# Performance work log

Hardware: AMD Instinct MI355X
Metric: run time of the kernel (lower is better)

The kernel has to match this reference:

```python
import jax, jax.numpy as jnp
import numpy as np

N_NODES = 100000
N_EDGES = 1600000
IN_CH = 128
OUT_CH = 128


def setup_inputs() -> dict:
    key = jax.random.key(0)
    k = jax.random.split(key, 6)
    x = jax.random.normal(k[0], (N_NODES, IN_CH), dtype=jnp.float32)
    edge_index = jax.random.randint(k[1], (2, N_EDGES), 0, N_NODES, dtype=jnp.int32)
    # GCNConv linear weights (glorot-ish scale) and biases
    W1 = jax.random.normal(k[2], (IN_CH, OUT_CH), dtype=jnp.float32) / np.sqrt(IN_CH)
    b1 = jnp.zeros((OUT_CH,), dtype=jnp.float32)
    W2 = jax.random.normal(k[3], (OUT_CH, OUT_CH), dtype=jnp.float32) / np.sqrt(OUT_CH)
    b2 = jnp.zeros((OUT_CH,), dtype=jnp.float32)
    return {"x": x, "edge_index": edge_index, "W1": W1, "b1": b1, "W2": W2, "b2": b2}


def gcn_conv(x, src, dst, W, b, n_nodes):
    """PyG GCNConv: add self-loops, symmetric D^-1/2 A D^-1/2 normalization."""
    h = x @ W  # [N, out]
    # degree including the implicit self-loop (weight 1)
    ones = jnp.ones(src.shape[0], dtype=x.dtype)
    deg = jax.ops.segment_sum(ones, dst, num_segments=n_nodes) + 1.0  # [N]
    dinv = jax.lax.rsqrt(deg)  # deg >= 1 so always finite
    coef = dinv[src] * dinv[dst]  # [E] edge norm 1/sqrt(d_i d_j)
    msg = h[src] * coef[:, None]  # [E, out] gather + scale
    agg = jax.ops.segment_sum(msg, dst, num_segments=n_nodes)  # scatter-add
    # self-loop contribution: norm = dinv[i]^2
    agg = agg + h * (dinv * dinv)[:, None]
    return agg + b


def reference(x, edge_index, W1, b1, W2, b2):
    src, dst = edge_index[0], edge_index[1]
    h = jax.nn.relu(gcn_conv(x, src, dst, W1, b1, N_NODES))
    out = jax.nn.relu(gcn_conv(h, src, dst, W2, b2, N_NODES))
    return out
```

## Files before the change

kernel.cpp:

```cpp
#include <hip/hip_runtime.h>


#define NN 100000
#define NBKT 512
#define BKT_W 196
#define CHUNK 8192
#define CAP 6144

typedef __attribute__((ext_vector_type(8))) short bf16x8;
typedef __attribute__((ext_vector_type(4))) float f32x4;

__device__ __forceinline__ ushort f2bf(float f) {
  unsigned u = __float_as_uint(f);
  unsigned r = (u + 0x7fffu + ((u >> 16) & 1u)) >> 16;
  return (ushort)r;
}
__device__ __forceinline__ float bflo(unsigned p) {
  return __uint_as_float(p << 16);
}
__device__ __forceinline__ float bfhi(unsigned p) {
  return __uint_as_float(p & 0xffff0000u);
}
__device__ __forceinline__ unsigned hipair(unsigned ue, unsigned uo) {
  return (uo & 0xffff0000u) | (ue >> 16);
}


__global__ __launch_bounds__(512) void kb_hist(const int* __restrict__ dst,
                                               int* __restrict__ bcnt, int E) {
  __shared__ int h[NBKT];
  for (int i = threadIdx.x; i < NBKT; i += 512) h[i] = 0;
  __syncthreads();
  int base = blockIdx.x * CHUNK;
#pragma unroll 4
  for (int q = 0; q < CHUNK / 512; q++) {
    int e = base + threadIdx.x + q * 512;
    if (e < E) atomicAdd(&h[dst[e] / BKT_W], 1);
  }
  __syncthreads();
  for (int i = threadIdx.x; i < NBKT; i += 512)
    if (h[i]) atomicAdd(&bcnt[i], h[i]);
}

__global__ __launch_bounds__(512) void kb_scan(const int* __restrict__ bcnt,
                                               int* __restrict__ bbase,
                                               int* __restrict__ bcur,
                                               int* __restrict__ row_ptr,
                                               int N, int E) {
  __shared__ int s[NBKT];
  int t = threadIdx.x;
  int v = bcnt[t];
  s[t] = v;
  __syncthreads();
  for (int off = 1; off < NBKT; off <<= 1) {
    int x = (t >= off) ? s[t - off] : 0;
    __syncthreads();
    s[t] += x;
    __syncthreads();
  }
  int ex = s[t] - v;
  bbase[t] = ex;
  bcur[t] = ex;
  if (t == NBKT - 1) bbase[NBKT] = E;
  if (t == 0) row_ptr[N] = E;
}

__global__ __launch_bounds__(512) void kb_scatter(const int* __restrict__ src,
                                                  const int* __restrict__ dst,
                                                  int* __restrict__ bcur,
                                                  int2* __restrict__ pairs, int E) {
  __shared__ int h[NBKT];
  __shared__ int gb[NBKT];
  for (int i = threadIdx.x; i < NBKT; i += 512) h[i] = 0;
  __syncthreads();

  const int base = blockIdx.x * CHUNK;
  const int t = threadIdx.x;
  int rank[CHUNK / 512], bkt[CHUNK / 512], sv[CHUNK / 512], dv[CHUNK / 512];
#pragma unroll
  for (int q = 0; q < CHUNK / 512; q++) {
    int e = base + t + q * 512;
    if (e < E) {
      int d = dst[e];
      int b = d / BKT_W;
      bkt[q] = b;
      sv[q] = src[e];
      dv[q] = d;
      rank[q] = atomicAdd(&h[b], 1);
    } else {
      bkt[q] = -1;
    }
  }
  __syncthreads();
  for (int i = t; i < NBKT; i += 512) {
    int c = h[i];
    gb[i] = c ? atomicAdd(&bcur[i], c) : 0;
  }
  __syncthreads();
#pragma unroll
  for (int q = 0; q < CHUNK / 512; q++) {
    if (bkt[q] >= 0) pairs[(size_t)gb[bkt[q]] + rank[q]] = make_int2(sv[q], dv[q]);
  }
}

__global__ __launch_bounds__(512) void kb_sort(const int* __restrict__ bbase,
                                               const int2* __restrict__ pairs,
                                               int* __restrict__ csr_src,
                                               int* __restrict__ row_ptr,
                                               float* __restrict__ dinv,
                                               int N, int E) {
  __shared__ int cnt[256];
  __shared__ int sc[256];
  __shared__ int cur[256];
  __shared__ int stage[CAP];

  const int b = blockIdx.x;
  const int t = threadIdx.x;
  const int lo = bbase[b], hi = bbase[b + 1];
  const int n0 = b * BKT_W;
  int m = hi - lo;
  if (m > CAP) m = CAP;

  if (t < 256) cnt[t] = 0;
  __syncthreads();

  for (int i = t; i < m; i += 512) {
    int2 p = pairs[(size_t)lo + i];
    atomicAdd(&cnt[p.y - n0], 1);
  }
  __syncthreads();

  int v = 0;
  if (t < 256) {
    v = cnt[t];
    sc[t] = v;
  }
  __syncthreads();
  for (int off = 1; off < 256; off <<= 1) {
    int x = 0;
    if (t < 256 && t >= off) x = sc[t - off];
    __syncthreads();
    if (t < 256) sc[t] += x;
    __syncthreads();
  }
  if (t < 256) {
    int ex = sc[t] - v;
    cur[t] = ex;
    int node = n0 + t;
    if (t < BKT_W && node < N) {
      row_ptr[node] = lo + ex;
      dinv[node] = rsqrtf((float)v + 1.0f);
    }
  }
  __syncthreads();

  for (int i = t; i < m; i += 512) {
    int2 p = pairs[(size_t)lo + i];
    int pos = atomicAdd(&cur[p.y - n0], 1);
    stage[pos] = p.x;
  }
  __syncthreads();

  for (int i = t; i < m; i += 512) csr_src[(size_t)lo + i] = stage[i];
}

__global__ __launch_bounds__(256) void k_wsplit2(const float* __restrict__ W1,
                                                 const float* __restrict__ W2,
                                                 ushort* __restrict__ w1hi,
                                                 ushort* __restrict__ w1lo,
                                                 ushort* __restrict__ w2hi,
                                                 ushort* __restrict__ w2lo) {
  const float* W = blockIdx.x ? W2 : W1;
  ushort* whi = blockIdx.x ? w2hi : w1hi;
  ushort* wlo = blockIdx.x ? w2lo : w1lo;
  const int t = threadIdx.x;
#pragma unroll
  for (int it = 0; it < 16; ++it) {
    int f4 = it * 256 + t;
    int k = f4 >> 5;
    int n4 = (f4 & 31) * 4;
    float4 v = *(const float4*)(W + (size_t)k * 128 + n4);
    float f[4] = {v.x, v.y, v.z, v.w};
#pragma unroll
    for (int q = 0; q < 4; ++q) {
      int n = n4 + q;
      unsigned u = __float_as_uint(f[q]);
      float lf = f[q] - __uint_as_float(u & 0xffff0000u);
      int bo = (n * 256 + k * 2) ^ ((n & 7) << 4);
      *(ushort*)((char*)whi + bo) = (ushort)(u >> 16);
      *(ushort*)((char*)wlo + bo) = (ushort)(__float_as_uint(lf) >> 16);
    }
  }
}

__device__ __forceinline__ void cvt_row(const float* __restrict__ p,
                                        bf16x8* hi, bf16x8* lo) {
  float4 v0 = *(const float4*)p;
  float4 v1 = *(const float4*)(p + 4);
  float f[8] = {v0.x, v0.y, v0.z, v0.w, v1.x, v1.y, v1.z, v1.w};
  unsigned hw[4], lw[4];
#pragma unroll
  for (int i = 0; i < 4; ++i) {
    unsigned u0 = __float_as_uint(f[2 * i]);
    unsigned u1 = __float_as_uint(f[2 * i + 1]);
    float l0 = f[2 * i] - __uint_as_float(u0 & 0xffff0000u);
    float l1 = f[2 * i + 1] - __uint_as_float(u1 & 0xffff0000u);
    hw[i] = hipair(u0, u1);
    lw[i] = hipair(__float_as_uint(l0), __float_as_uint(l1));
  }
  uint4 H = make_uint4(hw[0], hw[1], hw[2], hw[3]);
  uint4 L = make_uint4(lw[0], lw[1], lw[2], lw[3]);
  *hi = __builtin_bit_cast(bf16x8, H);
  *lo = __builtin_bit_cast(bf16x8, L);
}

__global__ __launch_bounds__(256) void k_gemm_mfma(const float* __restrict__ X,
                                                   const ushort* __restrict__ whi,
                                                   const ushort* __restrict__ wlo,
                                                   const float* __restrict__ dinv,
                                                   ushort* __restrict__ hs, int M) {
  __shared__ ushort wt_hi[128 * 128];
  __shared__ ushort wt_lo[128 * 128];

  const int t = threadIdx.x;
#pragma unroll
  for (int it = 0; it < 8; ++it) {
    int o = (it * 256 + t) * 8;
    *(uint4*)&wt_hi[o] = *(const uint4*)&whi[o];
    *(uint4*)&wt_lo[o] = *(const uint4*)&wlo[o];
  }
  __syncthreads();

  const int wv = t >> 6;
  const int lane = t & 63;
  const int r0 = blockIdx.x * 128 + wv * 32;
  const int la = lane & 15;
  const int kg = (lane >> 4) * 8;
  const int rowA = min(r0 + la, M - 1);
  const int rowB = min(r0 + 16 + la, M - 1);

  f32x4 acc[2][8];
#pragma unroll
  for (int rs = 0; rs < 2; ++rs)
#pragma unroll
    for (int ct = 0; ct < 8; ++ct) acc[rs][ct] = (f32x4)(0.f);

#pragma unroll
  for (int ks = 0; ks < 4; ++ks) {
    const int koff = ks * 32 + kg;
    bf16x8 ah0, al0, ah1, al1;
    cvt_row(X + (size_t)rowA * 128 + koff, &ah0, &al0);
    cvt_row(X + (size_t)rowB * 128 + koff, &ah1, &al1);
#pragma unroll
    for (int ct = 0; ct < 8; ++ct) {
      const int n = ct * 16 + la;
      const int bo = (n * 256 + koff * 2) ^ ((n & 7) << 4);
      bf16x8 bh = *(const bf16x8*)((const char*)wt_hi + bo);
      bf16x8 bl = *(const bf16x8*)((const char*)wt_lo + bo);
      acc[0][ct] = __builtin_amdgcn_mfma_f32_16x16x32_bf16(ah0, bh, acc[0][ct], 0, 0, 0);
      acc[0][ct] = __builtin_amdgcn_mfma_f32_16x16x32_bf16(ah0, bl, acc[0][ct], 0, 0, 0);
      acc[0][ct] = __builtin_amdgcn_mfma_f32_16x16x32_bf16(al0, bh, acc[0][ct], 0, 0, 0);
      acc[1][ct] = __builtin_amdgcn_mfma_f32_16x16x32_bf16(ah1, bh, acc[1][ct], 0, 0, 0);
      acc[1][ct] = __builtin_amdgcn_mfma_f32_16x16x32_bf16(ah1, bl, acc[1][ct], 0, 0, 0);
      acc[1][ct] = __builtin_amdgcn_mfma_f32_16x16x32_bf16(al1, bh, acc[1][ct], 0, 0, 0);
    }
  }

#pragma unroll
  for (int rs = 0; rs < 2; ++rs) {
#pragma unroll
    for (int j = 0; j < 4; ++j) {
      int r = r0 + rs * 16 + (lane >> 4) * 4 + j;
      if (r < M) {
        float sc = dinv[r];
#pragma unroll
        for (int ct = 0; ct < 8; ++ct)
          hs[(size_t)r * 128 + ct * 16 + la] = f2bf(acc[rs][ct][j] * sc);
      }
    }
  }
}

__global__ __launch_bounds__(256) void k_gemm_mfma_bf(const ushort* __restrict__ Xb,
                                                      const ushort* __restrict__ whi,
                                                      const ushort* __restrict__ wlo,
                                                      const float* __restrict__ dinv,
                                                      ushort* __restrict__ hs, int M) {
  __shared__ ushort wt_hi[128 * 128];
  __shared__ ushort wt_lo[128 * 128];

  const int t = threadIdx.x;
#pragma unroll
  for (int it = 0; it < 8; ++it) {
    int o = (it * 256 + t) * 8;
    *(uint4*)&wt_hi[o] = *(const uint4*)&whi[o];
    *(uint4*)&wt_lo[o] = *(const uint4*)&wlo[o];
  }
  __syncthreads();

  const int wv = t >> 6;
  const int lane = t & 63;
  const int r0 = blockIdx.x * 128 + wv * 32;
  const int la = lane & 15;
  const int kg = (lane >> 4) * 8;
  const int rowA = min(r0 + la, M - 1);
  const int rowB = min(r0 + 16 + la, M - 1);

  f32x4 acc[2][8];
#pragma unroll
  for (int rs = 0; rs < 2; ++rs)
#pragma unroll
    for (int ct = 0; ct < 8; ++ct) acc[rs][ct] = (f32x4)(0.f);

#pragma unroll
  for (int ks = 0; ks < 4; ++ks) {
    const int koff = ks * 32 + kg;
    bf16x8 a0 = *(const bf16x8*)(Xb + (size_t)rowA * 128 + koff);
    bf16x8 a1 = *(const bf16x8*)(Xb + (size_t)rowB * 128 + koff);
#pragma unroll
    for (int ct = 0; ct < 8; ++ct) {
      const int n = ct * 16 + la;
      const int bo = (n * 256 + koff * 2) ^ ((n & 7) << 4);
      bf16x8 bh = *(const bf16x8*)((const char*)wt_hi + bo);
      bf16x8 bl = *(const bf16x8*)((const char*)wt_lo + bo);
      acc[0][ct] = __builtin_amdgcn_mfma_f32_16x16x32_bf16(a0, bh, acc[0][ct], 0, 0, 0);
      acc[0][ct] = __builtin_amdgcn_mfma_f32_16x16x32_bf16(a0, bl, acc[0][ct], 0, 0, 0);
      acc[1][ct] = __builtin_amdgcn_mfma_f32_16x16x32_bf16(a1, bh, acc[1][ct], 0, 0, 0);
      acc[1][ct] = __builtin_amdgcn_mfma_f32_16x16x32_bf16(a1, bl, acc[1][ct], 0, 0, 0);
    }
  }

#pragma unroll
  for (int rs = 0; rs < 2; ++rs) {
#pragma unroll
    for (int j = 0; j < 4; ++j) {
      int r = r0 + rs * 16 + (lane >> 4) * 4 + j;
      if (r < M) {
        float sc = dinv[r];
#pragma unroll
        for (int ct = 0; ct < 8; ++ct)
          hs[(size_t)r * 128 + ct * 16 + la] = f2bf(acc[rs][ct][j] * sc);
      }
    }
  }
}

template <int BF16OUT>
__global__ __launch_bounds__(256) void k_agg(const int* __restrict__ row_ptr,
                                             const int* __restrict__ csr_src,
                                             const float* __restrict__ dinv,
                                             const ushort* __restrict__ hs,
                                             const float* __restrict__ bias,
                                             void* __restrict__ outv, int N) {
  const int node = blockIdx.x * 4 + (threadIdx.x >> 6);
  if (node >= N) return;
  const int lane = threadIdx.x & 63;
  const int qg = lane >> 4;
  const int cx = lane & 15;
  const uint4* hp = (const uint4*)hs;

  const int e0 = row_ptr[node];
  const int e1 = row_ptr[node + 1];

  float a[8];
#pragma unroll
  for (int i = 0; i < 8; ++i) a[i] = 0.f;

  int e = e0 + qg;
  for (; e + 4 < e1; e += 8) {
    int s0 = csr_src[e];
    int s1 = csr_src[e + 4];
    uint4 v0 = hp[(size_t)s0 * 16 + cx];
    uint4 v1 = hp[(size_t)s1 * 16 + cx];
    a[0] += bflo(v0.x) + bflo(v1.x);
    a[1] += bfhi(v0.x) + bfhi(v1.x);
    a[2] += bflo(v0.y) + bflo(v1.y);
    a[3] += bfhi(v0.y) + bfhi(v1.y);
    a[4] += bflo(v0.z) + bflo(v1.z);
    a[5] += bfhi(v0.z) + bfhi(v1.z);
    a[6] += bflo(v0.w) + bflo(v1.w);
    a[7] += bfhi(v0.w) + bfhi(v1.w);
  }
  for (; e < e1; e += 4) {
    int s = csr_src[e];
    uint4 v = hp[(size_t)s * 16 + cx];
    a[0] += bflo(v.x);
    a[1] += bfhi(v.x);
    a[2] += bflo(v.y);
    a[3] += bfhi(v.y);
    a[4] += bflo(v.z);
    a[5] += bfhi(v.z);
    a[6] += bflo(v.w);
    a[7] += bfhi(v.w);
  }
#pragma unroll
  for (int i = 0; i < 8; ++i) {
    a[i] += __shfl_xor(a[i], 16);
    a[i] += __shfl_xor(a[i], 32);
  }

  if (qg == 0) {
    uint4 sv = hp[(size_t)node * 16 + cx];
    a[0] += bflo(sv.x);
    a[1] += bfhi(sv.x);
    a[2] += bflo(sv.y);
    a[3] += bfhi(sv.y);
    a[4] += bflo(sv.z);
    a[5] += bfhi(sv.z);
    a[6] += bflo(sv.w);
    a[7] += bfhi(sv.w);
    float dv = dinv[node];
    float4 b0 = ((const float4*)bias)[cx * 2];
    float4 b1 = ((const float4*)bias)[cx * 2 + 1];
    float o[8];
    o[0] = fmaxf(fmaf(a[0], dv, b0.x), 0.f);
    o[1] = fmaxf(fmaf(a[1], dv, b0.y), 0.f);
    o[2] = fmaxf(fmaf(a[2], dv, b0.z), 0.f);
    o[3] = fmaxf(fmaf(a[3], dv, b0.w), 0.f);
    o[4] = fmaxf(fmaf(a[4], dv, b1.x), 0.f);
    o[5] = fmaxf(fmaf(a[5], dv, b1.y), 0.f);
    o[6] = fmaxf(fmaf(a[6], dv, b1.z), 0.f);
    o[7] = fmaxf(fmaf(a[7], dv, b1.w), 0.f);
    if (BF16OUT) {
      ushort u[8];
#pragma unroll
      for (int i = 0; i < 8; ++i) u[i] = f2bf(o[i]);
      ((uint4*)outv)[(size_t)node * 16 + cx] = *(const uint4*)u;
    } else {
      float4* op = (float4*)outv;
      op[(size_t)node * 32 + cx * 2] = make_float4(o[0], o[1], o[2], o[3]);
      op[(size_t)node * 32 + cx * 2 + 1] = make_float4(o[4], o[5], o[6], o[7]);
    }
  }
}


extern "C" void kernel_launch(void* const* d_in, const int* in_sizes, int n_in,
                              void* d_out, int out_size, void* d_ws, size_t ws_size,
                              hipStream_t stream) {
  const float* x  = (const float*)d_in[0];
  const int*   ei = (const int*)d_in[1];
  const float* W1 = (const float*)d_in[2];
  const float* b1 = (const float*)d_in[3];
  const float* W2 = (const float*)d_in[4];
  const float* b2 = (const float*)d_in[5];
  float* out = (float*)d_out;

  const int N = NN;
  const int E = in_sizes[1] / 2;
  const int* src = ei;
  const int* dst = ei + E;

  char* w = (char*)d_ws;
  auto alloc = [&](size_t bytes) {
    char* p = w;
    w += (bytes + 255) & ~(size_t)255;
    return p;
  };
  float*  dinv    = (float*)alloc((size_t)N * 4);
  int*    row_ptr = (int*)alloc((size_t)(N + 1) * 4);
  int*    bcnt    = (int*)alloc(NBKT * 4);
  int*    bbase   = (int*)alloc((NBKT + 1) * 4);
  int*    bcur    = (int*)alloc(NBKT * 4);
  int*    csr_src = (int*)alloc((size_t)E * 4);
  int2*   pairs   = (int2*)alloc((size_t)E * 8);
  ushort* hs      = (ushort*)alloc((size_t)N * 128 * 2);
  ushort* h1b     = (ushort*)alloc((size_t)N * 128 * 2);
  ushort* w1hi    = (ushort*)alloc(128 * 128 * 2);
  ushort* w1lo    = (ushort*)alloc(128 * 128 * 2);
  ushort* w2hi    = (ushort*)alloc(128 * 128 * 2);
  ushort* w2lo    = (ushort*)alloc(128 * 128 * 2);

  const int EB = (E + CHUNK - 1) / CHUNK;

  hipMemsetAsync(bcnt, 0, NBKT * 4, stream);
  kb_hist<<<EB, 512, 0, stream>>>(dst, bcnt, E);
  kb_scan<<<1, 512, 0, stream>>>(bcnt, bbase, bcur, row_ptr, N, E);
  kb_scatter<<<EB, 512, 0, stream>>>(src, dst, bcur, pairs, E);
  kb_sort<<<NBKT, 512, 0, stream>>>(bbase, pairs, csr_src, row_ptr, dinv, N, E);
  k_wsplit2<<<2, 256, 0, stream>>>(W1, W2, w1hi, w1lo, w2hi, w2lo);

  const int GB = (N + 127) / 128;
  const int AB = (N + 3) / 4;

  k_gemm_mfma<<<GB, 256, 0, stream>>>(x, w1hi, w1lo, dinv, hs, N);
  k_agg<1><<<AB, 256, 0, stream>>>(row_ptr, csr_src, dinv, hs, b1, h1b, N);
  k_gemm_mfma_bf<<<GB, 256, 0, stream>>>(h1b, w2hi, w2lo, dinv, hs, N);
  k_agg<0><<<AB, 256, 0, stream>>>(row_ptr, csr_src, dinv, hs, b2, out, N);
}
```

Measured before the change: 336.6 us.

## Pack edge pairs into 32-bit words, fuse weight split, truncate layer-1 input to bf16

The bucket-scatter pairs are packed into one 32-bit word (8-bit local dst, 24-bit src), which halves the traffic of the intermediate pairs array in scatter and sort. The weight hi/lo split kernel is folded into extra blocks of the histogram kernel to save a launch. The first GEMM now converts x to bf16 by truncation, keeping only the hi part and dropping the lo-part MFMAs, which cuts MFMA work but lowers precision. Packing assumes source indices fit in 24 bits and the in-bucket offset fits in 8 bits.

```diff
diff --git a/kernel.cpp b/kernel.cpp
--- a/kernel.cpp
+++ b/kernel.cpp
@@ -26,19 +26,47 @@
 }
 
 
-__global__ __launch_bounds__(512) void kb_hist(const int* __restrict__ dst,
-                                               int* __restrict__ bcnt, int E) {
+__global__ __launch_bounds__(512) void kb_hist_wsplit(
+    const int* __restrict__ dst, int* __restrict__ bcnt, int E, int EB,
+    const float* __restrict__ W1, const float* __restrict__ W2,
+    ushort* __restrict__ w1hi, ushort* __restrict__ w1lo,
+    ushort* __restrict__ w2hi, ushort* __restrict__ w2lo) {
+  const int t = threadIdx.x;
+  if ((int)blockIdx.x >= EB) {
+    const int wsel = blockIdx.x - EB;
+    const float* W = wsel ? W2 : W1;
+    ushort* whi = wsel ? w2hi : w1hi;
+    ushort* wlo = wsel ? w2lo : w1lo;
+#pragma unroll
+    for (int it = 0; it < 8; ++it) {
+      int f4 = it * 512 + t;
+      int k = f4 >> 5;
+      int n4 = (f4 & 31) * 4;
+      float4 v = *(const float4*)(W + (size_t)k * 128 + n4);
+      float f[4] = {v.x, v.y, v.z, v.w};
+#pragma unroll
+      for (int q = 0; q < 4; ++q) {
+        int n = n4 + q;
+        unsigned u = __float_as_uint(f[q]);
+        float lf = f[q] - __uint_as_float(u & 0xffff0000u);
+        int bo = (n * 256 + k * 2) ^ ((n & 7) << 4);
+        *(ushort*)((char*)whi + bo) = (ushort)(u >> 16);
+        *(ushort*)((char*)wlo + bo) = (ushort)(__float_as_uint(lf) >> 16);
+      }
+    }
+    return;
+  }
   __shared__ int h[NBKT];
-  for (int i = threadIdx.x; i < NBKT; i += 512) h[i] = 0;
+  for (int i = t; i < NBKT; i += 512) h[i] = 0;
   __syncthreads();
   int base = blockIdx.x * CHUNK;
 #pragma unroll 4
   for (int q = 0; q < CHUNK / 512; q++) {
-    int e = base + threadIdx.x + q * 512;
+    int e = base + t + q * 512;
     if (e < E) atomicAdd(&h[dst[e] / BKT_W], 1);
   }
   __syncthreads();
-  for (int i = threadIdx.x; i < NBKT; i += 512)
+  for (int i = t; i < NBKT; i += 512)
     if (h[i]) atomicAdd(&bcnt[i], h[i]);
 }
 
@@ -68,7 +96,7 @@
 __global__ __launch_bounds__(512) void kb_scatter(const int* __restrict__ src,
                                                   const int* __restrict__ dst,
                                                   int* __restrict__ bcur,
-                                                  int2* __restrict__ pairs, int E) {
+                                                  unsigned* __restrict__ pairs, int E) {
   __shared__ int h[NBKT];
   __shared__ int gb[NBKT];
   for (int i = threadIdx.x; i < NBKT; i += 512) h[i] = 0;
@@ -76,7 +104,8 @@
 
   const int base = blockIdx.x * CHUNK;
   const int t = threadIdx.x;
-  int rank[CHUNK / 512], bkt[CHUNK / 512], sv[CHUNK / 512], dv[CHUNK / 512];
+  int rank[CHUNK / 512], bkt[CHUNK / 512];
+  unsigned pv[CHUNK / 512];
 #pragma unroll
   for (int q = 0; q < CHUNK / 512; q++) {
     int e = base + t + q * 512;
@@ -84,8 +113,7 @@
       int d = dst[e];
       int b = d / BKT_W;
       bkt[q] = b;
-      sv[q] = src[e];
-      dv[q] = d;
+      pv[q] = ((unsigned)(d - b * BKT_W) << 24) | (unsigned)src[e];
       rank[q] = atomicAdd(&h[b], 1);
     } else {
       bkt[q] = -1;
@@ -99,12 +127,12 @@
   __syncthreads();
 #pragma unroll
   for (int q = 0; q < CHUNK / 512; q++) {
-    if (bkt[q] >= 0) pairs[(size_t)gb[bkt[q]] + rank[q]] = make_int2(sv[q], dv[q]);
+    if (bkt[q] >= 0) pairs[(size_t)gb[bkt[q]] + rank[q]] = pv[q];
   }
 }
 
 __global__ __launch_bounds__(512) void kb_sort(const int* __restrict__ bbase,
-                                               const int2* __restrict__ pairs,
+                                               const unsigned* __restrict__ pairs,
                                                int* __restrict__ csr_src,
                                                int* __restrict__ row_ptr,
                                                float* __restrict__ dinv,
@@ -125,8 +153,8 @@
   __syncthreads();
 
   for (int i = t; i < m; i += 512) {
-    int2 p = pairs[(size_t)lo + i];
-    atomicAdd(&cnt[p.y - n0], 1);
+    unsigned p = pairs[(size_t)lo + i];
+    atomicAdd(&cnt[p >> 24], 1);
   }
   __syncthreads();
 
@@ -155,70 +183,21 @@
   __syncthreads();
 
   for (int i = t; i < m; i += 512) {
-    int2 p = pairs[(size_t)lo + i];
-    int pos = atomicAdd(&cur[p.y - n0], 1);
-    stage[pos] = p.x;
+    unsigned p = pairs[(size_t)lo + i];
+    int pos = atomicAdd(&cur[p >> 24], 1);
+    stage[pos] = (int)(p & 0xFFFFFFu);
   }
   __syncthreads();
 
   for (int i = t; i < m; i += 512) csr_src[(size_t)lo + i] = stage[i];
 }
 
-__global__ __launch_bounds__(256) void k_wsplit2(const float* __restrict__ W1,
-                                                 const float* __restrict__ W2,
-                                                 ushort* __restrict__ w1hi,
-                                                 ushort* __restrict__ w1lo,
-                                                 ushort* __restrict__ w2hi,
-                                                 ushort* __restrict__ w2lo) {
-  const float* W = blockIdx.x ? W2 : W1;
-  ushort* whi = blockIdx.x ? w2hi : w1hi;
-  ushort* wlo = blockIdx.x ? w2lo : w1lo;
-  const int t = threadIdx.x;
-#pragma unroll
-  for (int it = 0; it < 16; ++it) {
-    int f4 = it * 256 + t;
-    int k = f4 >> 5;
-    int n4 = (f4 & 31) * 4;
-    float4 v = *(const float4*)(W + (size_t)k * 128 + n4);
-    float f[4] = {v.x, v.y, v.z, v.w};
-#pragma unroll
-    for (int q = 0; q < 4; ++q) {
-      int n = n4 + q;
-      unsigned u = __float_as_uint(f[q]);
-      float lf = f[q] - __uint_as_float(u & 0xffff0000u);
-      int bo = (n * 256 + k * 2) ^ ((n & 7) << 4);
-      *(ushort*)((char*)whi + bo) = (ushort)(u >> 16);
-      *(ushort*)((char*)wlo + bo) = (ushort)(__float_as_uint(lf) >> 16);
-    }
-  }
-}
-
-__device__ __forceinline__ void cvt_row(const float* __restrict__ p,
-                                        bf16x8* hi, bf16x8* lo) {
-  float4 v0 = *(const float4*)p;
-  float4 v1 = *(const float4*)(p + 4);
-  float f[8] = {v0.x, v0.y, v0.z, v0.w, v1.x, v1.y, v1.z, v1.w};
-  unsigned hw[4], lw[4];
-#pragma unroll
-  for (int i = 0; i < 4; ++i) {
-    unsigned u0 = __float_as_uint(f[2 * i]);
-    unsigned u1 = __float_as_uint(f[2 * i + 1]);
-    float l0 = f[2 * i] - __uint_as_float(u0 & 0xffff0000u);
-    float l1 = f[2 * i + 1] - __uint_as_float(u1 & 0xffff0000u);
-    hw[i] = hipair(u0, u1);
-    lw[i] = hipair(__float_as_uint(l0), __float_as_uint(l1));
-  }
-  uint4 H = make_uint4(hw[0], hw[1], hw[2], hw[3]);
-  uint4 L = make_uint4(lw[0], lw[1], lw[2], lw[3]);
-  *hi = __builtin_bit_cast(bf16x8, H);
-  *lo = __builtin_bit_cast(bf16x8, L);
-}
-
-__global__ __launch_bounds__(256) void k_gemm_mfma(const float* __restrict__ X,
-                                                   const ushort* __restrict__ whi,
-                                                   const ushort* __restrict__ wlo,
-                                                   const float* __restrict__ dinv,
-                                                   ushort* __restrict__ hs, int M) {
+template <int F32IN>
+__global__ __launch_bounds__(256) void k_gemm(const void* __restrict__ Xv,
+                                              const ushort* __restrict__ whi,
+                                              const ushort* __restrict__ wlo,
+                                              const float* __restrict__ dinv,
+                                              ushort* __restrict__ hs, int M) {
   __shared__ ushort wt_hi[128 * 128];
   __shared__ ushort wt_lo[128 * 128];
 
@@ -248,75 +227,28 @@
 #pragma unroll
   for (int ks = 0; ks < 4; ++ks) {
     const int koff = ks * 32 + kg;
-    bf16x8 ah0, al0, ah1, al1;
-    cvt_row(X + (size_t)rowA * 128 + koff, &ah0, &al0);
-    cvt_row(X + (size_t)rowB * 128 + koff, &ah1, &al1);
-#pragma unroll
-    for (int ct = 0; ct < 8; ++ct) {
-      const int n = ct * 16 + la;
-      const int bo = (n * 256 + koff * 2) ^ ((n & 7) << 4);
-      bf16x8 bh = *(const bf16x8*)((const char*)wt_hi + bo);
-      bf16x8 bl = *(const bf16x8*)((const char*)wt_lo + bo);
-      acc[0][ct] = __builtin_amdgcn_mfma_f32_16x16x32_bf16(ah0, bh, acc[0][ct], 0, 0, 0);
-      acc[0][ct] = __builtin_amdgcn_mfma_f32_16x16x32_bf16(ah0, bl, acc[0][ct], 0, 0, 0);
-      acc[0][ct] = __builtin_amdgcn_mfma_f32_16x16x32_bf16(al0, bh, acc[0][ct], 0, 0, 0);
-      acc[1][ct] = __builtin_amdgcn_mfma_f32_16x16x32_bf16(ah1, bh, acc[1][ct], 0, 0, 0);
-      acc[1][ct] = __builtin_amdgcn_mfma_f32_16x16x32_bf16(ah1, bl, acc[1][ct], 0, 0, 0);
-      acc[1][ct] = __builtin_amdgcn_mfma_f32_16x16x32_bf16(al1, bh, acc[1][ct], 0, 0, 0);
-    }
-  }
-
-#pragma unroll
-  for (int rs = 0; rs < 2; ++rs) {
-#pragma unroll
-    for (int j = 0; j < 4; ++j) {
-      int r = r0 + rs * 16 + (lane >> 4) * 4 + j;
-      if (r < M) {
-        float sc = dinv[r];
-#pragma unroll
-        for (int ct = 0; ct < 8; ++ct)
-          hs[(size_t)r * 128 + ct * 16 + la] = f2bf(acc[rs][ct][j] * sc);
-      }
-    }
-  }
-}
-
-__global__ __launch_bounds__(256) void k_gemm_mfma_bf(const ushort* __restrict__ Xb,
-                                                      const ushort* __restrict__ whi,
-                                                      const ushort* __restrict__ wlo,
-                                                      const float* __restrict__ dinv,
-                                                      ushort* __restrict__ hs, int M) {
-  __shared__ ushort wt_hi[128 * 128];
-  __shared__ ushort wt_lo[128 * 128];
-
-  const int t = threadIdx.x;
-#pragma unroll
-  for (int it = 0; it < 8; ++it) {
-    int o = (it * 256 + t) * 8;
-    *(uint4*)&wt_hi[o] = *(const uint4*)&whi[o];
-    *(uint4*)&wt_lo[o] = *(const uint4*)&wlo[o];
-  }
-  __syncthreads();
-
-  const int wv = t >> 6;
-  const int lane = t & 63;
-  const int r0 = blockIdx.x * 128 + wv * 32;
-  const int la = lane & 15;
-  const int kg = (lane >> 4) * 8;
-  const int rowA = min(r0 + la, M - 1);
-  const int rowB = min(r0 + 16 + la, M - 1);
-
-  f32x4 acc[2][8];
-#pragma unroll
-  for (int rs = 0; rs < 2; ++rs)
-#pragma unroll
-    for (int ct = 0; ct < 8; ++ct) acc[rs][ct] = (f32x4)(0.f);
-
-#pragma unroll
-  for (int ks = 0; ks < 4; ++ks) {
-    const int koff = ks * 32 + kg;
-    bf16x8 a0 = *(const bf16x8*)(Xb + (size_t)rowA * 128 + koff);
-    bf16x8 a1 = *(const bf16x8*)(Xb + (size_t)rowB * 128 + koff);
+    bf16x8 a0, a1;
+    if (F32IN) {
+      const float* pA = (const float*)Xv + (size_t)rowA * 128 + koff;
+      const float* pB = (const float*)Xv + (size_t)rowB * 128 + koff;
+      float4 u0 = *(const float4*)pA, u1 = *(const float4*)(pA + 4);
+      float4 v0 = *(const float4*)pB, v1 = *(const float4*)(pB + 4);
+      uint4 H0 = make_uint4(
+          hipair(__float_as_uint(u0.x), __float_as_uint(u0.y)),
+          hipair(__float_as_uint(u0.z), __float_as_uint(u0.w)),
+          hipair(__float_as_uint(u1.x), __float_as_uint(u1.y)),
+          hipair(__float_as_uint(u1.z), __float_as_uint(u1.w)));
+      uint4 H1 = make_uint4(
+          hipair(__float_as_uint(v0.x), __float_as_uint(v0.y)),
+          hipair(__float_as_uint(v0.z), __float_as_uint(v0.w)),
+          hipair(__float_as_uint(v1.x), __float_as_uint(v1.y)),
+          hipair(__float_as_uint(v1.z), __float_as_uint(v1.w)));
+      a0 = __builtin_bit_cast(bf16x8, H0);
+      a1 = __builtin_bit_cast(bf16x8, H1);
+    } else {
+      a0 = *(const bf16x8*)((const ushort*)Xv + (size_t)rowA * 128 + koff);
+      a1 = *(const bf16x8*)((const ushort*)Xv + (size_t)rowB * 128 + koff);
+    }
 #pragma unroll
     for (int ct = 0; ct < 8; ++ct) {
       const int n = ct * 16 + la;
@@ -457,34 +389,34 @@
     w += (bytes + 255) & ~(size_t)255;
     return p;
   };
-  float*  dinv    = (float*)alloc((size_t)N * 4);
-  int*    row_ptr = (int*)alloc((size_t)(N + 1) * 4);
-  int*    bcnt    = (int*)alloc(NBKT * 4);
-  int*    bbase   = (int*)alloc((NBKT + 1) * 4);
-  int*    bcur    = (int*)alloc(NBKT * 4);
-  int*    csr_src = (int*)alloc((size_t)E * 4);
-  int2*   pairs   = (int2*)alloc((size_t)E * 8);
-  ushort* hs      = (ushort*)alloc((size_t)N * 128 * 2);
-  ushort* h1b     = (ushort*)alloc((size_t)N * 128 * 2);
-  ushort* w1hi    = (ushort*)alloc(128 * 128 * 2);
-  ushort* w1lo    = (ushort*)alloc(128 * 128 * 2);
-  ushort* w2hi    = (ushort*)alloc(128 * 128 * 2);
-  ushort* w2lo    = (ushort*)alloc(128 * 128 * 2);
+  float*    dinv    = (float*)alloc((size_t)N * 4);
+  int*      row_ptr = (int*)alloc((size_t)(N + 1) * 4);
+  int*      bcnt    = (int*)alloc(NBKT * 4);
+  int*      bbase   = (int*)alloc((NBKT + 1) * 4);
+  int*      bcur    = (int*)alloc(NBKT * 4);
+  int*      csr_src = (int*)alloc((size_t)E * 4);
+  unsigned* pairs   = (unsigned*)alloc((size_t)E * 4);
+  ushort*   hs      = (ushort*)alloc((size_t)N * 128 * 2);
+  ushort*   h1b     = (ushort*)alloc((size_t)N * 128 * 2);
+  ushort*   w1hi    = (ushort*)alloc(128 * 128 * 2);
+  ushort*   w1lo    = (ushort*)alloc(128 * 128 * 2);
+  ushort*   w2hi    = (ushort*)alloc(128 * 128 * 2);
+  ushort*   w2lo    = (ushort*)alloc(128 * 128 * 2);
 
   const int EB = (E + CHUNK - 1) / CHUNK;
 
   hipMemsetAsync(bcnt, 0, NBKT * 4, stream);
-  kb_hist<<<EB, 512, 0, stream>>>(dst, bcnt, E);
+  kb_hist_wsplit<<<EB + 2, 512, 0, stream>>>(dst, bcnt, E, EB, W1, W2,
+                                             w1hi, w1lo, w2hi, w2lo);
   kb_scan<<<1, 512, 0, stream>>>(bcnt, bbase, bcur, row_ptr, N, E);
   kb_scatter<<<EB, 512, 0, stream>>>(src, dst, bcur, pairs, E);
   kb_sort<<<NBKT, 512, 0, stream>>>(bbase, pairs, csr_src, row_ptr, dinv, N, E);
-  k_wsplit2<<<2, 256, 0, stream>>>(W1, W2, w1hi, w1lo, w2hi, w2lo);
 
   const int GB = (N + 127) / 128;
   const int AB = (N + 3) / 4;
 
-  k_gemm_mfma<<<GB, 256, 0, stream>>>(x, w1hi, w1lo, dinv, hs, N);
+  k_gemm<1><<<GB, 256, 0, stream>>>(x, w1hi, w1lo, dinv, hs, N);
   k_agg<1><<<AB, 256, 0, stream>>>(row_ptr, csr_src, dinv, hs, b1, h1b, N);
-  k_gemm_mfma_bf<<<GB, 256, 0, stream>>>(h1b, w2hi, w2lo, dinv, hs, N);
+  k_gemm<0><<<GB, 256, 0, stream>>>(h1b, w2hi, w2lo, dinv, hs, N);
   k_agg<0><<<AB, 256, 0, stream>>>(row_ptr, csr_src, dinv, hs, b2, out, N);
 }
```

New measurement: 316.4 us. -6.0%, faster.
